# Kernel optimization log

Hardware: AMD Instinct MI355X
Metric: run time of the kernel (lower is better)

Reference implementation:

```python
import jax, jax.numpy as jnp
import numpy as np

N, E, F = 32768, 131072, 32

# (l_in, l_edge, l_out, op_type) for each of the 12 active paths; index = row of W
PATHS = [
    (0, 0, 0, 'prod'), (0, 1, 1, 'prod'), (0, 2, 2, 'prod'),
    (1, 0, 1, 'prod'), (2, 0, 2, 'prod'),
    (1, 1, 0, 'dot'), (1, 1, 1, 'cross'), (1, 1, 2, 'outer'),
    (2, 1, 1, 'mat_vec'), (1, 2, 1, 'vec_mat'),
    (2, 2, 0, 'double_dot'), (2, 2, 2, 'mat_mul_sym'),
]


def setup_inputs() -> dict:
    key = jax.random.key(0)
    ks = jax.random.split(key, 8)
    return {
        'h0': jax.random.normal(ks[0], (N, F), jnp.float32),
        'h1': jax.random.normal(ks[1], (N, 3, F), jnp.float32),
        'h2': jax.random.normal(ks[2], (N, 3, 3, F), jnp.float32),
        'g0': jax.random.normal(ks[3], (E, F), jnp.float32),
        'g1': jax.random.normal(ks[4], (E, 3, F), jnp.float32),
        'g2': jax.random.normal(ks[5], (E, 3, 3, F), jnp.float32),
        'W': jax.random.normal(ks[6], (len(PATHS), F, F), jnp.float32) * (F ** -0.5),
        'src': jax.random.randint(ks[7], (E,), 0, N, jnp.int32).astype(jnp.int64),
    }


def _leibniz(h0, h1, h2, g0, g1, g2, W, src):
    inv_sqrt_f = h0.shape[-1] ** -0.5
    # gather source-node features once per l
    h = {0: h0[src], 1: h1[src], 2: h2[src]}
    g = {0: g0, 1: g1, 2: g2}
    eye = jnp.eye(3, dtype=h0.dtype)[None, :, :, None]  # [1,3,3,1]
    msgs = {0: [], 1: [], 2: []}
    for p, (li, le, lo, op) in enumerate(PATHS):
        # nn.Linear(F,F,bias=False): y = x @ W^T, applied on last (feature) axis
        ht = jnp.einsum('...f,gf->...g', h[li], W[p])
        geom = g[le]
        if op == 'prod':
            if li == 0 and le == 0:
                res = ht * geom
            elif li == 0 and le == 1:
                res = ht[:, None, :] * geom
            elif li == 0 and le == 2:
                res = ht[:, None, None, :] * geom
            elif li == 1 and le == 0:
                res = ht * geom[:, None, :]
            else:  # li == 2, le == 0
                res = ht * geom[:, None, None, :]
        elif op == 'dot':
            res = jnp.sum(ht * geom, axis=1)
        elif op == 'cross':
            res = jnp.cross(ht, geom, axisa=1, axisb=1, axisc=1)
        elif op == 'outer':
            outer = ht[:, :, None, :] * geom[:, None, :, :]  # [E,3,3,F]
            trace = jnp.einsum('eiif->ef', outer)
            res = outer - (1.0 / 3.0) * trace[:, None, None, :] * eye
        elif op == 'mat_vec':
            res = jnp.einsum('eijf,ejf->eif', ht, geom)
        elif op == 'vec_mat':
            res = jnp.einsum('eif,eijf->ejf', ht, geom)
        elif op == 'double_dot':
            res = jnp.sum(ht * geom, axis=(1, 2))
        else:  # mat_mul_sym
            raw = jnp.einsum('eikf,ekjf->eijf', ht, geom)
            sym = 0.5 * (raw + jnp.swapaxes(raw, 1, 2))
            trace = jnp.einsum('eiif->ef', sym)
            res = sym - (1.0 / 3.0) * trace[:, None, None, :] * eye
        msgs[lo].append(res * inv_sqrt_f)
    return tuple(sum(msgs[l]) for l in (0, 1, 2))


def reference(h0, h1, h2, g0, g1, g2, W, src):
    return _leibniz(h0, h1, h2, g0, g1, g2, W, src)
```

## Files before the change

### kernel.cpp

```cpp
#include <hip/hip_runtime.h>

typedef float f32x4 __attribute__((ext_vector_type(4)));
typedef __bf16 bf16x8 __attribute__((ext_vector_type(8)));

constexpr float INV_SQRT_F = 0.17677669529663687f;

__device__ __forceinline__ f32x4 mfma16(bf16x8 a, bf16x8 b) {
  const f32x4 z = {0.f, 0.f, 0.f, 0.f};
  return __builtin_amdgcn_mfma_f32_16x16x32_bf16(a, b, z, 0, 0, 0);
}

__device__ __forceinline__ bf16x8 cvt_frag(f32x4 u, f32x4 v) {
  bf16x8 r;
  r[0] = (__bf16)u[0]; r[1] = (__bf16)u[1]; r[2] = (__bf16)u[2]; r[3] = (__bf16)u[3];
  r[4] = (__bf16)v[0]; r[5] = (__bf16)v[1]; r[6] = (__bf16)v[2]; r[7] = (__bf16)v[3];
  return r;
}

__device__ __forceinline__ f32x4 ld4(const float* __restrict__ p) {
  return *reinterpret_cast<const f32x4*>(p);
}

__global__ __launch_bounds__(256, 2)
void leibniz_fused(const float* __restrict__ h0, const float* __restrict__ h1,
                   const float* __restrict__ h2, const float* __restrict__ g0,
                   const float* __restrict__ g1, const float* __restrict__ g2,
                   const float* __restrict__ Wg, const int* __restrict__ src,
                   float* __restrict__ out, int E)
{
  __shared__ bf16x8 wlds[12 * 2 * 4 * 16];

  for (int c = threadIdx.x; c < 12 * 2 * 4 * 16; c += 256) {
    const int gl = c & 15;
    const int qq = (c >> 4) & 3;
    const int hf = (c >> 6) & 1;
    const int p  = c >> 7;
    const float* wp = Wg + (p * 32 + hf * 16 + gl) * 32 + qq * 8;
    bf16x8 f;
#pragma unroll
    for (int j = 0; j < 8; ++j) f[j] = (__bf16)(wp[j] * INV_SQRT_F);
    wlds[c] = f;
  }
  __syncthreads();

  const int lane = threadIdx.x & 63;
  const int wid  = threadIdx.x >> 6;
  const int eidx = lane & 15;
  const int q    = lane >> 4;
  int e0 = (blockIdx.x * 4 + wid) * 16;
  if (e0 > E - 16) e0 = E - 16;

  const int node = src[e0 + eidx];
  const int k0 = q * 8;

  const int e   = e0 + eidx;
  const int col = q * 4;
  const float* g0p = g0 + e * 32 + col;
  const float* g1p = g1 + (long long)e * 96 + col;
  const float* g2p = g2 + (long long)e * 288 + col;

  const float* h0p = h0 + node * 32 + k0;
  const float* h1p = h1 + node * 96 + k0;
  const float* h2p = h2 + (long long)node * 288 + k0;
  f32x4 r0a = ld4(h0p);
  f32x4 r0b = ld4(h0p + 4);
  f32x4 r1[6];
#pragma unroll
  for (int s = 0; s < 3; ++s) {
    r1[2 * s]     = ld4(h1p + s * 32);
    r1[2 * s + 1] = ld4(h1p + s * 32 + 4);
  }
  f32x4 r2[18];
#pragma unroll
  for (int s = 0; s < 9; ++s) {
    r2[2 * s]     = ld4(h2p + s * 32);
    r2[2 * s + 1] = ld4(h2p + s * 32 + 4);
  }

  f32x4 gv0[2];
  gv0[0] = ld4(g0p);
  gv0[1] = ld4(g0p + 16);
  f32x4 gv1[3][2];
#pragma unroll
  for (int s = 0; s < 3; ++s) {
    gv1[s][0] = ld4(g1p + s * 32);
    gv1[s][1] = ld4(g1p + s * 32 + 16);
  }

  const bf16x8 b0 = cvt_frag(r0a, r0b);
  bf16x8 b1[3];
#pragma unroll
  for (int s = 0; s < 3; ++s) b1[s] = cvt_frag(r1[2 * s], r1[2 * s + 1]);
  bf16x8 b2[9];
#pragma unroll
  for (int s = 0; s < 9; ++s) b2[s] = cvt_frag(r2[2 * s], r2[2 * s + 1]);

  f32x4 gkA[3][2], gkB[3][2];
#pragma unroll
  for (int j = 0; j < 3; ++j) {
    gkA[j][0] = ld4(g2p + j * 32);
    gkA[j][1] = ld4(g2p + j * 32 + 16);
  }
#pragma unroll
  for (int j = 0; j < 3; ++j) {
    gkB[j][0] = ld4(g2p + (3 + j) * 32);
    gkB[j][1] = ld4(g2p + (3 + j) * 32 + 16);
  }

  const f32x4 z4 = {0.f, 0.f, 0.f, 0.f};
  f32x4 acc0[2] = {z4, z4};
  f32x4 acc1[3][2];
  f32x4 acc2[9][2];
#pragma unroll
  for (int s = 0; s < 3; ++s) { acc1[s][0] = z4; acc1[s][1] = z4; }
#pragma unroll
  for (int s = 0; s < 9; ++s) { acc2[s][0] = z4; acc2[s][1] = z4; }

#define WFRAG(P, H) (wlds[(((P) * 2 + (H)) * 4 + q) * 16 + eidx])

#pragma unroll
  for (int h = 0; h < 2; ++h) {
    acc0[h] += mfma16(WFRAG(0, h), b0) * gv0[h];
    const bf16x8 w3 = WFRAG(3, h);
#pragma unroll
    for (int s = 0; s < 3; ++s) acc1[s][h] += mfma16(w3, b1[s]) * gv0[h];
    const bf16x8 w4 = WFRAG(4, h);
#pragma unroll
    for (int s = 0; s < 9; ++s) acc2[s][h] += mfma16(w4, b2[s]) * gv0[h];
  }

#pragma unroll
  for (int h = 0; h < 2; ++h) {
    {
      const f32x4 t = mfma16(WFRAG(1, h), b0);
#pragma unroll
      for (int s = 0; s < 3; ++s) acc1[s][h] += t * gv1[s][h];
    }
    {
      const bf16x8 w5 = WFRAG(5, h);
#pragma unroll
      for (int s = 0; s < 3; ++s) acc0[h] += mfma16(w5, b1[s]) * gv1[s][h];
    }
    {
      const bf16x8 w6 = WFRAG(6, h);
      const f32x4 c0 = mfma16(w6, b1[0]);
      const f32x4 c1 = mfma16(w6, b1[1]);
      const f32x4 c2 = mfma16(w6, b1[2]);
      acc1[0][h] += c1 * gv1[2][h] - c2 * gv1[1][h];
      acc1[1][h] += c2 * gv1[0][h] - c0 * gv1[2][h];
      acc1[2][h] += c0 * gv1[1][h] - c1 * gv1[0][h];
    }
    {
      const bf16x8 w7 = WFRAG(7, h);
      const f32x4 o0 = mfma16(w7, b1[0]);
      const f32x4 o1 = mfma16(w7, b1[1]);
      const f32x4 o2 = mfma16(w7, b1[2]);
      const f32x4 tr3 = (o0 * gv1[0][h] + o1 * gv1[1][h] + o2 * gv1[2][h]) * (1.f / 3.f);
      acc2[0][h] += o0 * gv1[0][h] - tr3;
      acc2[1][h] += o0 * gv1[1][h];
      acc2[2][h] += o0 * gv1[2][h];
      acc2[3][h] += o1 * gv1[0][h];
      acc2[4][h] += o1 * gv1[1][h] - tr3;
      acc2[5][h] += o1 * gv1[2][h];
      acc2[6][h] += o2 * gv1[0][h];
      acc2[7][h] += o2 * gv1[1][h];
      acc2[8][h] += o2 * gv1[2][h] - tr3;
    }
    {
      const bf16x8 w8 = WFRAG(8, h);
#pragma unroll
      for (int i = 0; i < 3; ++i)
#pragma unroll
        for (int j = 0; j < 3; ++j)
          acc1[i][h] += mfma16(w8, b2[i * 3 + j]) * gv1[j][h];
    }
  }

  f32x4 gkC[3][2];
#pragma unroll
  for (int j = 0; j < 3; ++j) {
    gkC[j][0] = ld4(g2p + (6 + j) * 32);
    gkC[j][1] = ld4(g2p + (6 + j) * 32 + 16);
  }

  f32x4 t2[2];
  t2[0] = mfma16(WFRAG(2, 0), b0);
  t2[1] = mfma16(WFRAG(2, 1), b0);

#define G2ROW_COMPUTE(K, GK)                                                   \
  {                                                                            \
    _Pragma("unroll")                                                          \
    for (int h = 0; h < 2; ++h) {                                              \
      _Pragma("unroll")                                                        \
      for (int j = 0; j < 3; ++j) acc2[(K) * 3 + j][h] += t2[h] * GK[j][h];    \
      {                                                                        \
        const f32x4 vk = mfma16(WFRAG(9, h), b1[(K)]);                         \
        _Pragma("unroll")                                                      \
        for (int j = 0; j < 3; ++j) acc1[j][h] += vk * GK[j][h];               \
      }                                                                        \
      {                                                                        \
        const bf16x8 w10 = WFRAG(10, h);                                       \
        _Pragma("unroll")                                                      \
        for (int j = 0; j < 3; ++j)                                            \
          acc0[h] += mfma16(w10, b2[(K) * 3 + j]) * GK[j][h];                  \
      }                                                                        \
      {                                                                        \
        const bf16x8 w11 = WFRAG(11, h);                                       \
        const f32x4 m0 = mfma16(w11, b2[0 * 3 + (K)]);                         \
        const f32x4 m1 = mfma16(w11, b2[1 * 3 + (K)]);                         \
        const f32x4 m2 = mfma16(w11, b2[2 * 3 + (K)]);                         \
        const f32x4 tk3 =                                                      \
            (m0 * GK[0][h] + m1 * GK[1][h] + m2 * GK[2][h]) * (1.f / 3.f);     \
        acc2[0][h] += m0 * GK[0][h] - tk3;                                     \
        acc2[4][h] += m1 * GK[1][h] - tk3;                                     \
        acc2[8][h] += m2 * GK[2][h] - tk3;                                     \
        const f32x4 s01 = (m0 * GK[1][h] + m1 * GK[0][h]) * 0.5f;              \
        acc2[1][h] += s01; acc2[3][h] += s01;                                  \
        const f32x4 s02 = (m0 * GK[2][h] + m2 * GK[0][h]) * 0.5f;              \
        acc2[2][h] += s02; acc2[6][h] += s02;                                  \
        const f32x4 s12 = (m1 * GK[2][h] + m2 * GK[1][h]) * 0.5f;              \
        acc2[5][h] += s12; acc2[7][h] += s12;                                  \
      }                                                                        \
    }                                                                          \
  }

  G2ROW_COMPUTE(0, gkA)
  G2ROW_COMPUTE(1, gkB)
  G2ROW_COMPUTE(2, gkC)

#undef G2ROW_COMPUTE

  float* o0p = out + (long long)e * 32 + col;
  float* o1p = out + (long long)E * 32 + (long long)e * 96 + col;
  float* o2p = out + (long long)E * 128 + (long long)e * 288 + col;

  *reinterpret_cast<f32x4*>(o0p)      = acc0[0];
  *reinterpret_cast<f32x4*>(o0p + 16) = acc0[1];
#pragma unroll
  for (int s = 0; s < 3; ++s) {
    *reinterpret_cast<f32x4*>(o1p + s * 32)      = acc1[s][0];
    *reinterpret_cast<f32x4*>(o1p + s * 32 + 16) = acc1[s][1];
  }
#pragma unroll
  for (int s = 0; s < 9; ++s) {
    *reinterpret_cast<f32x4*>(o2p + s * 32)      = acc2[s][0];
    *reinterpret_cast<f32x4*>(o2p + s * 32 + 16) = acc2[s][1];
  }
#undef WFRAG
}

extern "C" void kernel_launch(void* const* d_in, const int* in_sizes, int n_in,
                              void* d_out, int out_size, void* d_ws, size_t ws_size,
                              hipStream_t stream) {
  const float* h0 = (const float*)d_in[0];
  const float* h1 = (const float*)d_in[1];
  const float* h2 = (const float*)d_in[2];
  const float* g0 = (const float*)d_in[3];
  const float* g1 = (const float*)d_in[4];
  const float* g2 = (const float*)d_in[5];
  const float* Wg = (const float*)d_in[6];
  const int* src = (const int*)d_in[7];
  const int E = in_sizes[7];
  const int blocks = (E + 63) / 64;
  leibniz_fused<<<blocks, 256, 0, stream>>>(h0, h1, h2, g0, g1, g2, Wg, src,
                                            (float*)d_out, E);
}
```

Baseline: 142.4 us.

## Pre-convert node features and weights to bf16 in a prepass kernel

```diff
diff --git a/kernel.cpp b/kernel.cpp
--- a/kernel.cpp
+++ b/kernel.cpp
@@ -2,6 +2,7 @@
 
 typedef float f32x4 __attribute__((ext_vector_type(4)));
 typedef __bf16 bf16x8 __attribute__((ext_vector_type(8)));
+typedef __bf16 bf16x4 __attribute__((ext_vector_type(4)));
 
 constexpr float INV_SQRT_F = 0.17677669529663687f;
 
@@ -10,38 +11,66 @@
   return __builtin_amdgcn_mfma_f32_16x16x32_bf16(a, b, z, 0, 0, 0);
 }
 
-__device__ __forceinline__ bf16x8 cvt_frag(f32x4 u, f32x4 v) {
-  bf16x8 r;
-  r[0] = (__bf16)u[0]; r[1] = (__bf16)u[1]; r[2] = (__bf16)u[2]; r[3] = (__bf16)u[3];
-  r[4] = (__bf16)v[0]; r[5] = (__bf16)v[1]; r[6] = (__bf16)v[2]; r[7] = (__bf16)v[3];
-  return r;
-}
-
 __device__ __forceinline__ f32x4 ld4(const float* __restrict__ p) {
   return *reinterpret_cast<const f32x4*>(p);
 }
+__device__ __forceinline__ bf16x8 ldb8(const __bf16* __restrict__ p) {
+  return *reinterpret_cast<const bf16x8*>(p);
+}
+
+__global__ __launch_bounds__(256)
+void leibniz_prepass(const float* __restrict__ h0, const float* __restrict__ h1,
+                     const float* __restrict__ h2, const float* __restrict__ Wg,
+                     __bf16* __restrict__ ws, int n0, int n1, int n2)
+{
+  if (blockIdx.x == 0) {
+    bf16x8* wsW = reinterpret_cast<bf16x8*>(ws);
+    for (int c = threadIdx.x; c < 12 * 2 * 4 * 16; c += 256) {
+      const int gl = c & 15;
+      const int qq = (c >> 4) & 3;
+      const int hf = (c >> 6) & 1;
+      const int p  = c >> 7;
+      const float* wp = Wg + (p * 32 + hf * 16 + gl) * 32 + qq * 8;
+      bf16x8 f;
+#pragma unroll
+      for (int j = 0; j < 8; ++j) f[j] = (__bf16)(wp[j] * INV_SQRT_F);
+      wsW[c] = f;
+    }
+  }
+  __bf16* hb0 = ws + 12288;
+  __bf16* hb1 = hb0 + n0;
+  __bf16* hb2 = hb1 + n1;
+  const int q0 = n0 >> 2, q1 = n1 >> 2, q2 = n2 >> 2;
+  const int total = q0 + q1 + q2;
+  for (int i = blockIdx.x * 256 + threadIdx.x; i < total; i += gridDim.x * 256) {
+    const float* sp;
+    __bf16* dp;
+    if (i < q0)            { sp = h0 + 4 * i;              dp = hb0 + 4 * i; }
+    else if (i < q0 + q1)  { int j = i - q0;      sp = h1 + 4 * j; dp = hb1 + 4 * j; }
+    else                   { int j = i - q0 - q1; sp = h2 + 4 * j; dp = hb2 + 4 * j; }
+    const f32x4 v = *reinterpret_cast<const f32x4*>(sp);
+    bf16x4 o;
+    o[0] = (__bf16)v[0]; o[1] = (__bf16)v[1]; o[2] = (__bf16)v[2]; o[3] = (__bf16)v[3];
+    *reinterpret_cast<bf16x4*>(dp) = o;
+  }
+}
 
 __global__ __launch_bounds__(256, 2)
-void leibniz_fused(const float* __restrict__ h0, const float* __restrict__ h1,
-                   const float* __restrict__ h2, const float* __restrict__ g0,
-                   const float* __restrict__ g1, const float* __restrict__ g2,
-                   const float* __restrict__ Wg, const int* __restrict__ src,
-                   float* __restrict__ out, int E)
+void leibniz_fused_b(const __bf16* __restrict__ wsAll,
+                     const float* __restrict__ g0, const float* __restrict__ g1,
+                     const float* __restrict__ g2, const int* __restrict__ src,
+                     float* __restrict__ out, int E, int n0, int n1)
 {
   __shared__ bf16x8 wlds[12 * 2 * 4 * 16];
-
-  for (int c = threadIdx.x; c < 12 * 2 * 4 * 16; c += 256) {
-    const int gl = c & 15;
-    const int qq = (c >> 4) & 3;
-    const int hf = (c >> 6) & 1;
-    const int p  = c >> 7;
-    const float* wp = Wg + (p * 32 + hf * 16 + gl) * 32 + qq * 8;
-    bf16x8 f;
-#pragma unroll
-    for (int j = 0; j < 8; ++j) f[j] = (__bf16)(wp[j] * INV_SQRT_F);
-    wlds[c] = f;
+  {
+    const bf16x8* wsW = reinterpret_cast<const bf16x8*>(wsAll);
+    for (int c = threadIdx.x; c < 12 * 2 * 4 * 16; c += 256) wlds[c] = wsW[c];
   }
   __syncthreads();
+
+  const __bf16* hb0 = wsAll + 12288;
+  const __bf16* hb1 = hb0 + n0;
+  const __bf16* hb2 = hb1 + n1;
 
   const int lane = threadIdx.x & 63;
   const int wid  = threadIdx.x >> 6;
@@ -59,24 +88,6 @@
   const float* g1p = g1 + (long long)e * 96 + col;
   const float* g2p = g2 + (long long)e * 288 + col;
 
-  const float* h0p = h0 + node * 32 + k0;
-  const float* h1p = h1 + node * 96 + k0;
-  const float* h2p = h2 + (long long)node * 288 + k0;
-  f32x4 r0a = ld4(h0p);
-  f32x4 r0b = ld4(h0p + 4);
-  f32x4 r1[6];
-#pragma unroll
-  for (int s = 0; s < 3; ++s) {
-    r1[2 * s]     = ld4(h1p + s * 32);
-    r1[2 * s + 1] = ld4(h1p + s * 32 + 4);
-  }
-  f32x4 r2[18];
-#pragma unroll
-  for (int s = 0; s < 9; ++s) {
-    r2[2 * s]     = ld4(h2p + s * 32);
-    r2[2 * s + 1] = ld4(h2p + s * 32 + 4);
-  }
-
   f32x4 gv0[2];
   gv0[0] = ld4(g0p);
   gv0[1] = ld4(g0p + 16);
@@ -87,13 +98,13 @@
     gv1[s][1] = ld4(g1p + s * 32 + 16);
   }
 
-  const bf16x8 b0 = cvt_frag(r0a, r0b);
+  const bf16x8 b0 = ldb8(hb0 + node * 32 + k0);
   bf16x8 b1[3];
 #pragma unroll
-  for (int s = 0; s < 3; ++s) b1[s] = cvt_frag(r1[2 * s], r1[2 * s + 1]);
+  for (int s = 0; s < 3; ++s) b1[s] = ldb8(hb1 + node * 96 + s * 32 + k0);
   bf16x8 b2[9];
 #pragma unroll
-  for (int s = 0; s < 9; ++s) b2[s] = cvt_frag(r2[2 * s], r2[2 * s + 1]);
+  for (int s = 0; s < 9; ++s) b2[s] = ldb8(hb2 + (long long)node * 288 + s * 32 + k0);
 
   f32x4 gkA[3][2], gkB[3][2];
 #pragma unroll
@@ -174,13 +185,6 @@
         for (int j = 0; j < 3; ++j)
           acc1[i][h] += mfma16(w8, b2[i * 3 + j]) * gv1[j][h];
     }
-  }
-
-  f32x4 gkC[3][2];
-#pragma unroll
-  for (int j = 0; j < 3; ++j) {
-    gkC[j][0] = ld4(g2p + (6 + j) * 32);
-    gkC[j][1] = ld4(g2p + (6 + j) * 32 + 16);
   }
 
   f32x4 t2[2];
@@ -225,15 +229,230 @@
   }
 
   G2ROW_COMPUTE(0, gkA)
+
+#pragma unroll
+  for (int j = 0; j < 3; ++j) {
+    gkA[j][0] = ld4(g2p + (6 + j) * 32);
+    gkA[j][1] = ld4(g2p + (6 + j) * 32 + 16);
+  }
+
   G2ROW_COMPUTE(1, gkB)
-  G2ROW_COMPUTE(2, gkC)
-
+  G2ROW_COMPUTE(2, gkA)
 #undef G2ROW_COMPUTE
 
   float* o0p = out + (long long)e * 32 + col;
   float* o1p = out + (long long)E * 32 + (long long)e * 96 + col;
   float* o2p = out + (long long)E * 128 + (long long)e * 288 + col;
 
+  *reinterpret_cast<f32x4*>(o0p)      = acc0[0];
+  *reinterpret_cast<f32x4*>(o0p + 16) = acc0[1];
+#pragma unroll
+  for (int s = 0; s < 3; ++s) {
+    *reinterpret_cast<f32x4*>(o1p + s * 32)      = acc1[s][0];
+    *reinterpret_cast<f32x4*>(o1p + s * 32 + 16) = acc1[s][1];
+  }
+#pragma unroll
+  for (int s = 0; s < 9; ++s) {
+    *reinterpret_cast<f32x4*>(o2p + s * 32)      = acc2[s][0];
+    *reinterpret_cast<f32x4*>(o2p + s * 32 + 16) = acc2[s][1];
+  }
+#undef WFRAG
+}
+
+__device__ __forceinline__ bf16x8 cvt_frag(f32x4 u, f32x4 v) {
+  bf16x8 r;
+  r[0] = (__bf16)u[0]; r[1] = (__bf16)u[1]; r[2] = (__bf16)u[2]; r[3] = (__bf16)u[3];
+  r[4] = (__bf16)v[0]; r[5] = (__bf16)v[1]; r[6] = (__bf16)v[2]; r[7] = (__bf16)v[3];
+  return r;
+}
+
+__global__ __launch_bounds__(256, 2)
+void leibniz_fused_fb(const float* __restrict__ h0, const float* __restrict__ h1,
+                      const float* __restrict__ h2, const float* __restrict__ g0,
+                      const float* __restrict__ g1, const float* __restrict__ g2,
+                      const float* __restrict__ Wg, const int* __restrict__ src,
+                      float* __restrict__ out, int E)
+{
+  __shared__ bf16x8 wlds[12 * 2 * 4 * 16];
+  for (int c = threadIdx.x; c < 12 * 2 * 4 * 16; c += 256) {
+    const int gl = c & 15;
+    const int qq = (c >> 4) & 3;
+    const int hf = (c >> 6) & 1;
+    const int p  = c >> 7;
+    const float* wp = Wg + (p * 32 + hf * 16 + gl) * 32 + qq * 8;
+    bf16x8 f;
+#pragma unroll
+    for (int j = 0; j < 8; ++j) f[j] = (__bf16)(wp[j] * INV_SQRT_F);
+    wlds[c] = f;
+  }
+  __syncthreads();
+
+  const int lane = threadIdx.x & 63;
+  const int wid  = threadIdx.x >> 6;
+  const int eidx = lane & 15;
+  const int q    = lane >> 4;
+  int e0 = (blockIdx.x * 4 + wid) * 16;
+  if (e0 > E - 16) e0 = E - 16;
+
+  const int node = src[e0 + eidx];
+  const int k0 = q * 8;
+  const int e   = e0 + eidx;
+  const int col = q * 4;
+  const float* g0p = g0 + e * 32 + col;
+  const float* g1p = g1 + (long long)e * 96 + col;
+  const float* g2p = g2 + (long long)e * 288 + col;
+
+  const float* h0p = h0 + node * 32 + k0;
+  const float* h1p = h1 + node * 96 + k0;
+  const float* h2p = h2 + (long long)node * 288 + k0;
+  f32x4 r0a = ld4(h0p), r0b = ld4(h0p + 4);
+  f32x4 r1[6];
+#pragma unroll
+  for (int s = 0; s < 3; ++s) { r1[2*s] = ld4(h1p + s*32); r1[2*s+1] = ld4(h1p + s*32 + 4); }
+  f32x4 r2[18];
+#pragma unroll
+  for (int s = 0; s < 9; ++s) { r2[2*s] = ld4(h2p + s*32); r2[2*s+1] = ld4(h2p + s*32 + 4); }
+
+  f32x4 gv0[2];
+  gv0[0] = ld4(g0p); gv0[1] = ld4(g0p + 16);
+  f32x4 gv1[3][2];
+#pragma unroll
+  for (int s = 0; s < 3; ++s) { gv1[s][0] = ld4(g1p + s*32); gv1[s][1] = ld4(g1p + s*32 + 16); }
+
+  const bf16x8 b0 = cvt_frag(r0a, r0b);
+  bf16x8 b1[3];
+#pragma unroll
+  for (int s = 0; s < 3; ++s) b1[s] = cvt_frag(r1[2*s], r1[2*s+1]);
+  bf16x8 b2[9];
+#pragma unroll
+  for (int s = 0; s < 9; ++s) b2[s] = cvt_frag(r2[2*s], r2[2*s+1]);
+
+  f32x4 gkA[3][2], gkB[3][2];
+#pragma unroll
+  for (int j = 0; j < 3; ++j) { gkA[j][0] = ld4(g2p + j*32); gkA[j][1] = ld4(g2p + j*32 + 16); }
+#pragma unroll
+  for (int j = 0; j < 3; ++j) { gkB[j][0] = ld4(g2p + (3+j)*32); gkB[j][1] = ld4(g2p + (3+j)*32 + 16); }
+
+  const f32x4 z4 = {0.f, 0.f, 0.f, 0.f};
+  f32x4 acc0[2] = {z4, z4};
+  f32x4 acc1[3][2];
+  f32x4 acc2[9][2];
+#pragma unroll
+  for (int s = 0; s < 3; ++s) { acc1[s][0] = z4; acc1[s][1] = z4; }
+#pragma unroll
+  for (int s = 0; s < 9; ++s) { acc2[s][0] = z4; acc2[s][1] = z4; }
+
+#define WFRAG(P, H) (wlds[(((P) * 2 + (H)) * 4 + q) * 16 + eidx])
+#pragma unroll
+  for (int h = 0; h < 2; ++h) {
+    acc0[h] += mfma16(WFRAG(0, h), b0) * gv0[h];
+    const bf16x8 w3 = WFRAG(3, h);
+#pragma unroll
+    for (int s = 0; s < 3; ++s) acc1[s][h] += mfma16(w3, b1[s]) * gv0[h];
+    const bf16x8 w4 = WFRAG(4, h);
+#pragma unroll
+    for (int s = 0; s < 9; ++s) acc2[s][h] += mfma16(w4, b2[s]) * gv0[h];
+  }
+#pragma unroll
+  for (int h = 0; h < 2; ++h) {
+    {
+      const f32x4 t = mfma16(WFRAG(1, h), b0);
+#pragma unroll
+      for (int s = 0; s < 3; ++s) acc1[s][h] += t * gv1[s][h];
+    }
+    {
+      const bf16x8 w5 = WFRAG(5, h);
+#pragma unroll
+      for (int s = 0; s < 3; ++s) acc0[h] += mfma16(w5, b1[s]) * gv1[s][h];
+    }
+    {
+      const bf16x8 w6 = WFRAG(6, h);
+      const f32x4 c0 = mfma16(w6, b1[0]);
+      const f32x4 c1 = mfma16(w6, b1[1]);
+      const f32x4 c2 = mfma16(w6, b1[2]);
+      acc1[0][h] += c1 * gv1[2][h] - c2 * gv1[1][h];
+      acc1[1][h] += c2 * gv1[0][h] - c0 * gv1[2][h];
+      acc1[2][h] += c0 * gv1[1][h] - c1 * gv1[0][h];
+    }
+    {
+      const bf16x8 w7 = WFRAG(7, h);
+      const f32x4 o0 = mfma16(w7, b1[0]);
+      const f32x4 o1 = mfma16(w7, b1[1]);
+      const f32x4 o2 = mfma16(w7, b1[2]);
+      const f32x4 tr3 = (o0 * gv1[0][h] + o1 * gv1[1][h] + o2 * gv1[2][h]) * (1.f / 3.f);
+      acc2[0][h] += o0 * gv1[0][h] - tr3;
+      acc2[1][h] += o0 * gv1[1][h];
+      acc2[2][h] += o0 * gv1[2][h];
+      acc2[3][h] += o1 * gv1[0][h];
+      acc2[4][h] += o1 * gv1[1][h] - tr3;
+      acc2[5][h] += o1 * gv1[2][h];
+      acc2[6][h] += o2 * gv1[0][h];
+      acc2[7][h] += o2 * gv1[1][h];
+      acc2[8][h] += o2 * gv1[2][h] - tr3;
+    }
+    {
+      const bf16x8 w8 = WFRAG(8, h);
+#pragma unroll
+      for (int i = 0; i < 3; ++i)
+#pragma unroll
+        for (int j = 0; j < 3; ++j)
+          acc1[i][h] += mfma16(w8, b2[i * 3 + j]) * gv1[j][h];
+    }
+  }
+
+  f32x4 gkC[3][2];
+#pragma unroll
+  for (int j = 0; j < 3; ++j) { gkC[j][0] = ld4(g2p + (6+j)*32); gkC[j][1] = ld4(g2p + (6+j)*32 + 16); }
+
+  f32x4 t2[2];
+  t2[0] = mfma16(WFRAG(2, 0), b0);
+  t2[1] = mfma16(WFRAG(2, 1), b0);
+
+#define G2ROW_COMPUTE(K, GK)                                                   \
+  {                                                                            \
+    _Pragma("unroll")                                                          \
+    for (int h = 0; h < 2; ++h) {                                              \
+      _Pragma("unroll")                                                        \
+      for (int j = 0; j < 3; ++j) acc2[(K) * 3 + j][h] += t2[h] * GK[j][h];    \
+      {                                                                        \
+        const f32x4 vk = mfma16(WFRAG(9, h), b1[(K)]);                         \
+        _Pragma("unroll")                                                      \
+        for (int j = 0; j < 3; ++j) acc1[j][h] += vk * GK[j][h];               \
+      }                                                                        \
+      {                                                                        \
+        const bf16x8 w10 = WFRAG(10, h);                                       \
+        _Pragma("unroll")                                                      \
+        for (int j = 0; j < 3; ++j)                                            \
+          acc0[h] += mfma16(w10, b2[(K) * 3 + j]) * GK[j][h];                  \
+      }                                                                        \
+      {                                                                        \
+        const bf16x8 w11 = WFRAG(11, h);                                       \
+        const f32x4 m0 = mfma16(w11, b2[0 * 3 + (K)]);                         \
+        const f32x4 m1 = mfma16(w11, b2[1 * 3 + (K)]);                         \
+        const f32x4 m2 = mfma16(w11, b2[2 * 3 + (K)]);                         \
+        const f32x4 tk3 =                                                      \
+            (m0 * GK[0][h] + m1 * GK[1][h] + m2 * GK[2][h]) * (1.f / 3.f);     \
+        acc2[0][h] += m0 * GK[0][h] - tk3;                                     \
+        acc2[4][h] += m1 * GK[1][h] - tk3;                                     \
+        acc2[8][h] += m2 * GK[2][h] - tk3;                                     \
+        const f32x4 s01 = (m0 * GK[1][h] + m1 * GK[0][h]) * 0.5f;              \
+        acc2[1][h] += s01; acc2[3][h] += s01;                                  \
+        const f32x4 s02 = (m0 * GK[2][h] + m2 * GK[0][h]) * 0.5f;              \
+        acc2[2][h] += s02; acc2[6][h] += s02;                                  \
+        const f32x4 s12 = (m1 * GK[2][h] + m2 * GK[1][h]) * 0.5f;              \
+        acc2[5][h] += s12; acc2[7][h] += s12;                                  \
+      }                                                                        \
+    }                                                                          \
+  }
+
+  G2ROW_COMPUTE(0, gkA)
+  G2ROW_COMPUTE(1, gkB)
+  G2ROW_COMPUTE(2, gkC)
+#undef G2ROW_COMPUTE
+
+  float* o0p = out + (long long)e * 32 + col;
+  float* o1p = out + (long long)E * 32 + (long long)e * 96 + col;
+  float* o2p = out + (long long)E * 128 + (long long)e * 288 + col;
   *reinterpret_cast<f32x4*>(o0p)      = acc0[0];
   *reinterpret_cast<f32x4*>(o0p + 16) = acc0[1];
 #pragma unroll
@@ -261,7 +480,17 @@
   const float* Wg = (const float*)d_in[6];
   const int* src = (const int*)d_in[7];
   const int E = in_sizes[7];
+  const int n0 = in_sizes[0], n1 = in_sizes[1], n2 = in_sizes[2];
+  const size_t need = 24576 + (size_t)(n0 + n1 + n2) * 2;
   const int blocks = (E + 63) / 64;
-  leibniz_fused<<<blocks, 256, 0, stream>>>(h0, h1, h2, g0, g1, g2, Wg, src,
-                                            (float*)d_out, E);
-}
+
+  if (ws_size >= need) {
+    __bf16* ws = (__bf16*)d_ws;
+    leibniz_prepass<<<2048, 256, 0, stream>>>(h0, h1, h2, Wg, ws, n0, n1, n2);
+    leibniz_fused_b<<<blocks, 256, 0, stream>>>(ws, g0, g1, g2, src,
+                                                (float*)d_out, E, n0, n1);
+  } else {
+    leibniz_fused_fb<<<blocks, 256, 0, stream>>>(h0, h1, h2, g0, g1, g2, Wg, src,
+                                                 (float*)d_out, E);
+  }
+}
```

Result: slower. 188.1 us (+32.1%).
